# Kernel tuning notes

Hardware: AMD Instinct MI355X
Metric: run time of the kernel (lower is better)

The kernel has to match this reference:

```python
import jax, jax.numpy as jnp
import numpy as np

V, E, H, T = 50000, 300, 512, 16   # vocab, embed_dim, hidden_dim, tagset
Hh = H // 2                         # per-direction LSTM hidden
B, S = 128, 128                     # batch (hardcoded in module), seq_len
START, STOP = 14, 15
NEG = -10000.0


def setup_inputs() -> dict:
    key = jax.random.key(0)
    ks = jax.random.split(key, 16)
    n = lambda k, sh: (jax.random.normal(k, sh, dtype=jnp.float32) * 0.1)
    trans = jax.random.normal(ks[12], (T, T), dtype=jnp.float32)
    trans = trans.at[START, :].set(NEG).at[:, STOP].set(NEG)
    return {
        "sentence": jax.random.randint(ks[0], (B, S), 0, V, dtype=jnp.int32),
        "emb": jax.random.normal(ks[1], (V, E), dtype=jnp.float32),
        "Wih_f": n(ks[2], (4 * Hh, E)), "Whh_f": n(ks[3], (4 * Hh, Hh)),
        "bih_f": n(ks[4], (4 * Hh,)),   "bhh_f": n(ks[5], (4 * Hh,)),
        "Wih_b": n(ks[6], (4 * Hh, E)), "Whh_b": n(ks[7], (4 * Hh, Hh)),
        "bih_b": n(ks[8], (4 * Hh,)),   "bhh_b": n(ks[9], (4 * Hh,)),
        "W_out": n(ks[10], (T, H)),     "b_out": n(ks[11], (T,)),
        "trans": trans,
        "h0": jax.random.normal(ks[13], (2, B, Hh), dtype=jnp.float32),
        "c0": jax.random.normal(ks[14], (2, B, Hh), dtype=jnp.float32),
    }


def _lstm_dir(x_sbE, h0, c0, Wih, Whh, bih, bhh):
    """x_sbE: [S,B,E] -> [S,B,Hh]. PyTorch gate order: i,f,g,o."""
    def cell(carry, xt):
        h, c = carry
        g = xt @ Wih.T + bih + h @ Whh.T + bhh
        i, f, gg, o = jnp.split(g, 4, axis=-1)
        c = jax.nn.sigmoid(f) * c + jax.nn.sigmoid(i) * jnp.tanh(gg)
        h = jax.nn.sigmoid(o) * jnp.tanh(c)
        return (h, c), h
    _, hs = jax.lax.scan(cell, (h0, c0), x_sbE)
    return hs


def _viterbi(feats, trans):
    """Batched Viterbi. feats: [B,S,T]. Returns (scores [B], paths [B,S])."""
    init = jnp.full((B, T), NEG, dtype=feats.dtype).at[:, START].set(0.0)

    def step(fv, feat_t):
        # next_tag_var[b, next, prev] = fv[b, prev] + trans[next, prev]
        nxt = fv[:, None, :] + trans[None, :, :]
        bp = jnp.argmax(nxt, axis=-1)              # [B,T]
        fv = jnp.max(nxt, axis=-1) + feat_t        # [B,T]
        return fv, bp

    fv, bps = jax.lax.scan(step, init, jnp.swapaxes(feats, 0, 1))  # bps: [S,B,T]
    term = fv + trans[STOP][None, :]
    best = jnp.argmax(term, axis=-1)               # [B]
    score = jnp.max(term, axis=-1)                 # [B]

    def back(tag, bp_t):
        prev = jnp.take_along_axis(bp_t, tag[:, None], axis=1)[:, 0]
        return prev, tag

    _, path = jax.lax.scan(back, best, bps, reverse=True)  # [S,B]
    return score, jnp.swapaxes(path, 0, 1)


def reference(sentence, emb, Wih_f, Whh_f, bih_f, bhh_f,
              Wih_b, Whh_b, bih_b, bhh_b, W_out, b_out, trans, h0, c0):
    x = emb[sentence]                               # [B,S,E] (frozen embedding)
    x_sbE = jnp.swapaxes(x, 0, 1)                   # [S,B,E]
    h_f = _lstm_dir(x_sbE, h0[0], c0[0], Wih_f, Whh_f, bih_f, bhh_f)
    h_b = _lstm_dir(x_sbE[::-1], h0[1], c0[1], Wih_b, Whh_b, bih_b, bhh_b)[::-1]
    lstm_out = jnp.concatenate([h_f, h_b], axis=-1)  # [S,B,H]
    feats = jnp.swapaxes(lstm_out @ W_out.T + b_out, 0, 1)  # [B,S,T]
    scores, tag_seqs = _viterbi(feats, trans)
    return scores, tag_seqs
```

## Files before the change

kernel.cpp:

```cpp
#include <hip/hip_runtime.h>
#include <math.h>
#include <stdint.h>

#define BB 128
#define SS 128
#define EE 300
#define HH 256
#define G4 1024
#define TT 16
#define NEGV -10000.0f
#define START_TAG 14
#define STOP_TAG 15

typedef float f32x4 __attribute__((ext_vector_type(4)));
typedef int   i32x4 __attribute__((ext_vector_type(4)));

__device__ __forceinline__ float sigm(float x) { return 1.0f / (1.0f + expf(-x)); }

__device__ __forceinline__ float4 shfl_xor4(float4 v, int m) {
  float4 r;
  r.x = __shfl_xor(v.x, m); r.y = __shfl_xor(v.y, m);
  r.z = __shfl_xor(v.z, m); r.w = __shfl_xor(v.w, m);
  return r;
}
__device__ __forceinline__ void add4(float4& a, const float4& b) {
  a.x += b.x; a.y += b.y; a.z += b.z; a.w += b.w;
}

__device__ __forceinline__ f32x4 load_f4_llc(const float* p) {
  f32x4 v;
  asm volatile("global_load_dwordx4 %0, %1, off sc0 sc1\n\t"
               "s_waitcnt vmcnt(0)"
               : "=v"(v) : "v"(p) : "memory");
  return v;
}
__device__ __forceinline__ void load_tags8(const int* p, i32x4& a, i32x4& b) {
  asm volatile("global_load_dwordx4 %0, %2, off sc0 sc1\n\t"
               "global_load_dwordx4 %1, %2, off offset:16 sc0 sc1\n\t"
               "s_waitcnt vmcnt(0)"
               : "=&v"(a), "=&v"(b) : "v"(p) : "memory");
}

__global__ void k_prep(const float* __restrict__ Wih_f, const float* __restrict__ Whh_f,
                       const float* __restrict__ bih_f, const float* __restrict__ bhh_f,
                       const float* __restrict__ Wih_b, const float* __restrict__ Whh_b,
                       const float* __restrict__ bih_b, const float* __restrict__ bhh_b,
                       float* __restrict__ WihT, float* __restrict__ Whh4,
                       float* __restrict__ bsum, int* __restrict__ ctr) {
  int id = blockIdx.x * blockDim.x + threadIdx.x;
  const int N1 = 2 * EE * G4;
  const int N2 = 2 * HH * G4;
  const int N3 = 2 * G4;
  const int N4 = 64 * 256;
  if (id < N1) {
    int d = id / (EE * G4); int r = id % (EE * G4);
    int e = r / G4; int j = r % G4;
    const float* W = d ? Wih_b : Wih_f;
    WihT[id] = W[j * EE + e];
  } else if (id < N1 + N2) {
    int t = id - N1;
    int d = t / (HH * G4); int r = t % (HH * G4);
    int k = r / G4; int q = r % G4; int u = q >> 2; int g = q & 3;
    const float* W = d ? Whh_b : Whh_f;
    Whh4[t] = W[(g * HH + u) * HH + k];
  } else if (id < N1 + N2 + N3) {
    int t = id - N1 - N2;
    int d = t / G4; int j = t % G4;
    bsum[t] = d ? (bih_b[j] + bhh_b[j]) : (bih_f[j] + bhh_f[j]);
  } else if (id < N1 + N2 + N3 + N4) {
    ctr[id - N1 - N2 - N3] = 0;
  }
}

__global__ void k_xproj(const int* __restrict__ sent, const float* __restrict__ emb,
                        const float* __restrict__ WihT, const float* __restrict__ bsum,
                        float4* __restrict__ xp4) {
  __shared__ __align__(16) float xs[16][EE];
  __shared__ int idxs[16];
  int blk = blockIdx.x;
  int d = blk >> 10;
  int tile = blk & 1023;
  int tid = threadIdx.x;
  if (tid < 16) {
    int sb = tile * 16 + tid;
    int s = sb >> 7, b = sb & 127;
    idxs[tid] = sent[b * SS + s];
  }
  __syncthreads();
  for (int t = tid; t < 16 * 75; t += 256) {
    int i = t / 75, e4 = t % 75;
    ((f32x4*)&xs[i][0])[e4] = ((const f32x4*)(emb + (size_t)idxs[i] * EE))[e4];
  }
  __syncthreads();

  const float* WT = WihT + (size_t)d * EE * G4;
  float acc0[16], acc1[16], acc2[16], acc3[16];
#pragma unroll
  for (int i = 0; i < 16; ++i) { acc0[i] = 0.f; acc1[i] = 0.f; acc2[i] = 0.f; acc3[i] = 0.f; }

  for (int e4 = 0; e4 < 75; ++e4) {
    f32x4 xv[16];
#pragma unroll
    for (int i = 0; i < 16; ++i)
      xv[i] = *(const f32x4*)&xs[i][e4 * 4];
    const float* rowb = WT + (size_t)e4 * 4 * G4;
#pragma unroll
    for (int j = 0; j < 4; ++j) {
      const float* row = rowb + (size_t)j * G4;
      float w0 = row[tid];
      float w1 = row[tid + 256];
      float w2 = row[tid + 512];
      float w3 = row[tid + 768];
#pragma unroll
      for (int i = 0; i < 16; ++i) {
        float x = xv[i][j];
        acc0[i] += w0 * x; acc1[i] += w1 * x; acc2[i] += w2 * x; acc3[i] += w3 * x;
      }
    }
  }
  float b0 = bsum[d * G4 + tid];
  float b1 = bsum[d * G4 + tid + 256];
  float b2 = bsum[d * G4 + tid + 512];
  float b3 = bsum[d * G4 + tid + 768];
#pragma unroll
  for (int i = 0; i < 16; ++i) {
    int sb = tile * 16 + i;
    int s = sb >> 7, b = sb & 127;
    xp4[(((size_t)d * SS + s) * BB + b) * HH + tid] =
        make_float4(acc0[i] + b0, acc1[i] + b1, acc2[i] + b2, acc3[i] + b3);
  }
}

__global__ __launch_bounds__(256, 2) void k_recur(
    const float4* __restrict__ xp4, const float4* __restrict__ Wg,
    const float* __restrict__ Wout, const float* __restrict__ h0,
    const float* __restrict__ c0, float* __restrict__ hbuf,
    float* __restrict__ featsP, int* __restrict__ ctr) {
  __shared__ __align__(16) float hshS[4 * 288];
  __shared__ float hloc[4 * 33];
  __shared__ float WoL[16 * 33];

  int blk = blockIdx.x;
  int d = blk >> 8;
  int bg = (blk >> 3) & 31;
  int sl = blk & 7;
  int bbase = bg * 4;
  int tid = threadIdx.x;
  int u = tid >> 3, kc = tid & 7;
  int uglob = sl * 32 + u;
  int* tagsg = ctr + (d * 32 + bg) * 256 + 64;

  for (int i = tid; i < 16 * 32; i += 256) {
    int t = i >> 5, uu = i & 31;
    WoL[t * 33 + uu] = Wout[t * 512 + d * HH + sl * 32 + uu];
  }

  float4 wreg[32];
  {
    const float4* Wd = Wg + (size_t)d * (HH * HH) + (size_t)(kc * 32) * HH + uglob;
#pragma unroll
    for (int kk = 0; kk < 32; ++kk) wreg[kk] = Wd[(size_t)kk * HH];
  }
  int b_own = ((kc & 1) << 1) | ((kc >> 1) & 1);
  float c_reg = c0[((size_t)d * BB + bbase + b_own) * HH + uglob];
  bool up0 = (kc & 1), up1 = (kc & 2);

  int sb = tid >> 6;
  int sk = (tid & 63) * 4;
  int ldoff = sb * 288 + (sk >> 5) * 36 + (sk & 31);

  for (int step = 0; step < SS; ++step) {
    int s = d ? (SS - 1 - step) : step;
    float4 xg = xp4[(((size_t)d * SS + s) * BB + bbase + b_own) * HH + uglob];

    float* ldst = &hshS[ldoff];
    if (step == 0) {
      const float* ps = h0 + ((size_t)d * BB + bbase + sb) * HH + sk;
      *(f32x4*)ldst = *(const f32x4*)ps;
    } else {
      i32x4 ta, tb;
      int m;
      do {
        load_tags8(tagsg, ta, tb);
        int m0 = min(min(ta[0], ta[1]), min(ta[2], ta[3]));
        int m1 = min(min(tb[0], tb[1]), min(tb[2], tb[3]));
        m = min(m0, m1);
      } while (m < step);
      const float* ps = hbuf + ((size_t)((step - 1) % 3) * 2 + d) * BB * HH +
                        (size_t)(bbase + sb) * HH + sk;
      *(f32x4*)ldst = load_f4_llc(ps);
    }
    __syncthreads();

    float4 a[4];
#pragma unroll
    for (int b = 0; b < 4; ++b) a[b] = make_float4(0.f, 0.f, 0.f, 0.f);
#pragma unroll
    for (int kk4 = 0; kk4 < 8; ++kk4) {
      float hvv[4][4];
#pragma unroll
      for (int b = 0; b < 4; ++b)
        *(f32x4*)&hvv[b][0] = *(const f32x4*)&hshS[b * 288 + kc * 36 + kk4 * 4];
#pragma unroll
      for (int j = 0; j < 4; ++j) {
        float4 w = wreg[kk4 * 4 + j];
#pragma unroll
        for (int b = 0; b < 4; ++b) {
          float hj = hvv[b][j];
          a[b].x += w.x * hj; a[b].y += w.y * hj;
          a[b].z += w.z * hj; a[b].w += w.w * hj;
        }
      }
    }

#pragma unroll
    for (int j = 0; j < 2; ++j) {
      float4 snd = up0 ? a[j] : a[j + 2];
      float4 rcv = shfl_xor4(snd, 1);
      if (!up0) add4(a[j], rcv); else add4(a[j + 2], rcv);
    }
    float4 v0 = up0 ? a[2] : a[0];
    float4 v1 = up0 ? a[3] : a[1];
    {
      float4 snd = up1 ? v0 : v1;
      float4 rcv = shfl_xor4(snd, 2);
      if (!up1) add4(v0, rcv); else add4(v1, rcv);
    }
    float4 keep = up1 ? v1 : v0;
    {
      float4 rcv = shfl_xor4(keep, 4);
      add4(keep, rcv);
    }

    float ii = keep.x + xg.x, ff = keep.y + xg.y;
    float gg = keep.z + xg.z, oo = keep.w + xg.w;
    c_reg = sigm(ff) * c_reg + sigm(ii) * tanhf(gg);
    float hn = sigm(oo) * tanhf(c_reg);

    if (kc < 4) {
      __hip_atomic_store(
          &hbuf[((size_t)(step % 3) * 2 + d) * BB * HH + (size_t)(bbase + b_own) * HH + uglob],
          hn, __ATOMIC_RELAXED, __HIP_MEMORY_SCOPE_AGENT);
      hloc[b_own * 33 + u] = hn;
    }
    __syncthreads();

    if (tid == 0)
      __hip_atomic_store(&tagsg[sl], step + 1, __ATOMIC_RELAXED,
                         __HIP_MEMORY_SCOPE_AGENT);

    {
      int b2 = tid >> 6, t = (tid >> 2) & 15, pr = tid & 3;
      float p = 0.f;
#pragma unroll
      for (int q = 0; q < 8; ++q)
        p += hloc[b2 * 33 + pr * 8 + q] * WoL[t * 33 + pr * 8 + q];
      p += __shfl_xor(p, 1);
      p += __shfl_xor(p, 2);
      if (pr == 0)
        featsP[(((size_t)(d * 8 + sl) * BB + bbase + b2) * SS + s) * TT + t] = p;
    }
  }
}

__global__ void k_fsum(const float* __restrict__ featsP, float* __restrict__ featsF) {
  int b = blockIdx.x;
  int tid = threadIdx.x;
  float acc[8];
#pragma unroll
  for (int j = 0; j < 8; ++j) acc[j] = 0.f;
  for (int dsl = 0; dsl < 16; ++dsl) {
    const float* fp = featsP + ((size_t)dsl * BB + b) * (SS * TT);
#pragma unroll
    for (int j = 0; j < 8; ++j) acc[j] += fp[j * 256 + tid];
  }
  float* fo = featsF + (size_t)b * (SS * TT);
#pragma unroll
  for (int j = 0; j < 8; ++j) fo[j * 256 + tid] = acc[j];
}

__global__ void k_viterbi(const float* __restrict__ featsF, const float* __restrict__ b_out,
                          const float* __restrict__ trans, float* __restrict__ out) {
  __shared__ float tr[TT * TT];
  __shared__ unsigned char bpl[16][SS][TT];
  int tid = threadIdx.x;
  if (tid < TT * TT) tr[tid] = trans[tid];
  __syncthreads();

  int bg = tid >> 4;
  int next = tid & 15;
  int b = blockIdx.x * 16 + bg;
  float fv = (next == START_TAG) ? 0.0f : NEGV;
  float bo = b_out[next];
  const float* fF = featsF + (size_t)b * SS * TT;

  for (int s = 0; s < SS; ++s) {
    float best = -INFINITY; int arg = 0;
#pragma unroll
    for (int prev = 0; prev < TT; ++prev) {
      float fvp = __shfl(fv, prev, 16);
      float cand = fvp + tr[next * TT + prev];
      if (cand > best) { best = cand; arg = prev; }
    }
    float feat = fF[s * TT + next] + bo;
    fv = best + feat;
    bpl[bg][s][next] = (unsigned char)arg;
  }

  float bv = fv + tr[STOP_TAG * TT + next];
  int bi = next;
#pragma unroll
  for (int off = 8; off; off >>= 1) {
    float ov = __shfl_down(bv, off, 16);
    int oi = __shfl_down(bi, off, 16);
    if (ov > bv || (ov == bv && oi < bi)) { bv = ov; bi = oi; }
  }
  if (next == 0) {
    out[b] = bv;
    int tag = bi;
    float* po = out + BB + (size_t)b * SS;
    for (int s = SS - 1; s >= 0; --s) {
      po[s] = (float)tag;
      tag = bpl[bg][s][tag];
    }
  }
}

extern "C" void kernel_launch(void* const* d_in, const int* in_sizes, int n_in,
                              void* d_out, int out_size, void* d_ws, size_t ws_size,
                              hipStream_t stream) {
  const int*   sent  = (const int*)d_in[0];
  const float* emb   = (const float*)d_in[1];
  const float* Wih_f = (const float*)d_in[2];
  const float* Whh_f = (const float*)d_in[3];
  const float* bih_f = (const float*)d_in[4];
  const float* bhh_f = (const float*)d_in[5];
  const float* Wih_b = (const float*)d_in[6];
  const float* Whh_b = (const float*)d_in[7];
  const float* bih_b = (const float*)d_in[8];
  const float* bhh_b = (const float*)d_in[9];
  const float* Wout  = (const float*)d_in[10];
  const float* b_out = (const float*)d_in[11];
  const float* trans = (const float*)d_in[12];
  const float* h0    = (const float*)d_in[13];
  const float* c0    = (const float*)d_in[14];

  float* ws = (float*)d_ws;
  size_t off = 0;
  float* xproj  = ws + off; off += (size_t)2 * SS * BB * G4;
  float* WihT   = ws + off; off += (size_t)2 * EE * G4;
  float* Whh4   = ws + off; off += (size_t)2 * HH * G4;
  float* bsum   = ws + off; off += (size_t)2 * G4;
  float* featsP = ws + off; off += (size_t)16 * BB * SS * TT;
  float* featsF = ws + off; off += (size_t)BB * SS * TT;
  float* hbuf   = ws + off; off += (size_t)3 * 2 * BB * HH;
  int*   ctr    = (int*)(ws + off); off += 64 * 256;

  const int NPREP = 2 * EE * G4 + 2 * HH * G4 + 2 * G4 + 64 * 256;
  k_prep<<<(NPREP + 255) / 256, 256, 0, stream>>>(Wih_f, Whh_f, bih_f, bhh_f,
                                                  Wih_b, Whh_b, bih_b, bhh_b,
                                                  WihT, Whh4, bsum, ctr);
  k_xproj<<<2048, 256, 0, stream>>>(sent, emb, WihT, bsum, (float4*)xproj);

  {
    const float4* xp4c = (const float4*)xproj;
    const float4* Wgc  = (const float4*)Whh4;
    void* kargs[] = {(void*)&xp4c, (void*)&Wgc, (void*)&Wout, (void*)&h0,
                     (void*)&c0, (void*)&hbuf, (void*)&featsP, (void*)&ctr};
    hipError_t e = hipLaunchCooperativeKernel(k_recur, dim3(512), dim3(256),
                                              kargs, 0, stream);
    if (e != hipSuccess) {
      k_recur<<<512, 256, 0, stream>>>(xp4c, Wgc, Wout, h0, c0, hbuf, featsP, ctr);
    }
  }

  k_fsum<<<BB, 256, 0, stream>>>(featsP, featsF);
  k_viterbi<<<8, 256, 0, stream>>>(featsF, b_out, trans, (float*)d_out);
}
```

Baseline: 841.3 us.

## Replace tag-counter sync with stamped h-value pairs and move output projection out

Each hidden value is now stored together with its step stamp as one 64-bit atomic. Consumers spin on the stamps directly instead of first polling per-slice counters and then loading hbuf, which removes a round trip and a block barrier from the serial recurrence. The h tile in shared memory is double-buffered, which removes the second __syncthreads per step. The per-step output projection and the fsum pass are replaced by storing all h values and running a separate k_feats GEMV kernel, at the cost of extra memory traffic and one more kernel.

```diff
diff --git a/kernel.cpp b/kernel.cpp
--- a/kernel.cpp
+++ b/kernel.cpp
@@ -13,7 +13,6 @@
 #define STOP_TAG 15
 
 typedef float f32x4 __attribute__((ext_vector_type(4)));
-typedef int   i32x4 __attribute__((ext_vector_type(4)));
 
 __device__ __forceinline__ float sigm(float x) { return 1.0f / (1.0f + expf(-x)); }
 
@@ -27,18 +26,16 @@
   a.x += b.x; a.y += b.y; a.z += b.z; a.w += b.w;
 }
 
-__device__ __forceinline__ f32x4 load_f4_llc(const float* p) {
-  f32x4 v;
-  asm volatile("global_load_dwordx4 %0, %1, off sc0 sc1\n\t"
-               "s_waitcnt vmcnt(0)"
-               : "=v"(v) : "v"(p) : "memory");
-  return v;
-}
-__device__ __forceinline__ void load_tags8(const int* p, i32x4& a, i32x4& b) {
+__device__ __forceinline__ void load_pairs8(const float* p, f32x4& a, f32x4& b) {
   asm volatile("global_load_dwordx4 %0, %2, off sc0 sc1\n\t"
                "global_load_dwordx4 %1, %2, off offset:16 sc0 sc1\n\t"
                "s_waitcnt vmcnt(0)"
                : "=&v"(a), "=&v"(b) : "v"(p) : "memory");
+}
+
+__device__ __forceinline__ void store_pair_llc(float2* p, float h, int stamp) {
+  uint64_t bits = ((uint64_t)(uint32_t)stamp << 32) | (uint64_t)__float_as_uint(h);
+  __hip_atomic_store((uint64_t*)p, bits, __ATOMIC_RELAXED, __HIP_MEMORY_SCOPE_AGENT);
 }
 
 __global__ void k_prep(const float* __restrict__ Wih_f, const float* __restrict__ Whh_f,
@@ -46,12 +43,12 @@
                        const float* __restrict__ Wih_b, const float* __restrict__ Whh_b,
                        const float* __restrict__ bih_b, const float* __restrict__ bhh_b,
                        float* __restrict__ WihT, float* __restrict__ Whh4,
-                       float* __restrict__ bsum, int* __restrict__ ctr) {
+                       float* __restrict__ bsum, float* __restrict__ hpairz) {
   int id = blockIdx.x * blockDim.x + threadIdx.x;
   const int N1 = 2 * EE * G4;
   const int N2 = 2 * HH * G4;
   const int N3 = 2 * G4;
-  const int N4 = 64 * 256;
+  const int N4 = 3 * 2 * BB * HH * 2;
   if (id < N1) {
     int d = id / (EE * G4); int r = id % (EE * G4);
     int e = r / G4; int j = r % G4;
@@ -68,7 +65,7 @@
     int d = t / G4; int j = t % G4;
     bsum[t] = d ? (bih_b[j] + bhh_b[j]) : (bih_f[j] + bhh_f[j]);
   } else if (id < N1 + N2 + N3 + N4) {
-    ctr[id - N1 - N2 - N3] = 0;
+    hpairz[id - N1 - N2 - N3] = 0.0f;
   }
 }
 
@@ -133,12 +130,9 @@
 
 __global__ __launch_bounds__(256, 2) void k_recur(
     const float4* __restrict__ xp4, const float4* __restrict__ Wg,
-    const float* __restrict__ Wout, const float* __restrict__ h0,
-    const float* __restrict__ c0, float* __restrict__ hbuf,
-    float* __restrict__ featsP, int* __restrict__ ctr) {
-  __shared__ __align__(16) float hshS[4 * 288];
-  __shared__ float hloc[4 * 33];
-  __shared__ float WoL[16 * 33];
+    const float* __restrict__ h0, const float* __restrict__ c0,
+    float2* __restrict__ hpair, float* __restrict__ hall) {
+  __shared__ __align__(16) float hsh[2][4 * 288];
 
   int blk = blockIdx.x;
   int d = blk >> 8;
@@ -148,12 +142,6 @@
   int tid = threadIdx.x;
   int u = tid >> 3, kc = tid & 7;
   int uglob = sl * 32 + u;
-  int* tagsg = ctr + (d * 32 + bg) * 256 + 64;
-
-  for (int i = tid; i < 16 * 32; i += 256) {
-    int t = i >> 5, uu = i & 31;
-    WoL[t * 33 + uu] = Wout[t * 512 + d * HH + sl * 32 + uu];
-  }
 
   float4 wreg[32];
   {
@@ -166,32 +154,35 @@
   bool up0 = (kc & 1), up1 = (kc & 2);
 
   int sb = tid >> 6;
-  int sk = (tid & 63) * 4;
-  int ldoff = sb * 288 + (sk >> 5) * 36 + (sk & 31);
+  int k4 = (tid & 63) * 4;
+  int ldoff = sb * 288 + (k4 >> 5) * 36 + (k4 & 31);
 
   for (int step = 0; step < SS; ++step) {
     int s = d ? (SS - 1 - step) : step;
+    int pb = step & 1;
     float4 xg = xp4[(((size_t)d * SS + s) * BB + bbase + b_own) * HH + uglob];
 
-    float* ldst = &hshS[ldoff];
+    float* ldst = &hsh[pb][ldoff];
     if (step == 0) {
-      const float* ps = h0 + ((size_t)d * BB + bbase + sb) * HH + sk;
+      const float* ps = h0 + ((size_t)d * BB + bbase + sb) * HH + k4;
       *(f32x4*)ldst = *(const f32x4*)ps;
     } else {
-      i32x4 ta, tb;
-      int m;
-      do {
-        load_tags8(tagsg, ta, tb);
-        int m0 = min(min(ta[0], ta[1]), min(ta[2], ta[3]));
-        int m1 = min(min(tb[0], tb[1]), min(tb[2], tb[3]));
-        m = min(m0, m1);
-      } while (m < step);
-      const float* ps = hbuf + ((size_t)((step - 1) % 3) * 2 + d) * BB * HH +
-                        (size_t)(bbase + sb) * HH + sk;
-      *(f32x4*)ldst = load_f4_llc(ps);
+      int slot_r = (step + 2) % 3;
+      const float* ps = (const float*)(hpair +
+          ((size_t)(slot_r * 2 + d) * BB + bbase + sb) * HH + k4);
+      f32x4 v0, v1;
+      load_pairs8(ps, v0, v1);
+      while (__float_as_int(v0[1]) != step || __float_as_int(v0[3]) != step ||
+             __float_as_int(v1[1]) != step || __float_as_int(v1[3]) != step) {
+        __builtin_amdgcn_s_sleep(1);
+        load_pairs8(ps, v0, v1);
+      }
+      f32x4 q = {v0[0], v0[2], v1[0], v1[2]};
+      *(f32x4*)ldst = q;
     }
     __syncthreads();
 
+    const float* hb = &hsh[pb][0];
     float4 a[4];
 #pragma unroll
     for (int b = 0; b < 4; ++b) a[b] = make_float4(0.f, 0.f, 0.f, 0.f);
@@ -200,7 +191,7 @@
       float hvv[4][4];
 #pragma unroll
       for (int b = 0; b < 4; ++b)
-        *(f32x4*)&hvv[b][0] = *(const f32x4*)&hshS[b * 288 + kc * 36 + kk4 * 4];
+        *(f32x4*)&hvv[b][0] = *(const f32x4*)&hb[b * 288 + kc * 36 + kk4 * 4];
 #pragma unroll
       for (int j = 0; j < 4; ++j) {
         float4 w = wreg[kk4 * 4 + j];
@@ -238,45 +229,41 @@
     float hn = sigm(oo) * tanhf(c_reg);
 
     if (kc < 4) {
-      __hip_atomic_store(
-          &hbuf[((size_t)(step % 3) * 2 + d) * BB * HH + (size_t)(bbase + b_own) * HH + uglob],
-          hn, __ATOMIC_RELAXED, __HIP_MEMORY_SCOPE_AGENT);
-      hloc[b_own * 33 + u] = hn;
-    }
-    __syncthreads();
-
-    if (tid == 0)
-      __hip_atomic_store(&tagsg[sl], step + 1, __ATOMIC_RELAXED,
-                         __HIP_MEMORY_SCOPE_AGENT);
-
-    {
-      int b2 = tid >> 6, t = (tid >> 2) & 15, pr = tid & 3;
-      float p = 0.f;
-#pragma unroll
-      for (int q = 0; q < 8; ++q)
-        p += hloc[b2 * 33 + pr * 8 + q] * WoL[t * 33 + pr * 8 + q];
-      p += __shfl_xor(p, 1);
-      p += __shfl_xor(p, 2);
-      if (pr == 0)
-        featsP[(((size_t)(d * 8 + sl) * BB + bbase + b2) * SS + s) * TT + t] = p;
-    }
-  }
-}
-
-__global__ void k_fsum(const float* __restrict__ featsP, float* __restrict__ featsF) {
-  int b = blockIdx.x;
+      store_pair_llc(&hpair[((size_t)((step % 3) * 2 + d) * BB + bbase + b_own) * HH + uglob],
+                     hn, step + 1);
+      hall[(((size_t)d * SS + step) * BB + bbase + b_own) * HH + uglob] = hn;
+    }
+  }
+}
+
+__global__ void k_feats(const float* __restrict__ hall, const float* __restrict__ Wout,
+                        float* __restrict__ featsF) {
+  __shared__ __align__(16) float h2[16][516];
+  int b = blockIdx.x >> 3;
+  int sg = blockIdx.x & 7;
   int tid = threadIdx.x;
-  float acc[8];
-#pragma unroll
-  for (int j = 0; j < 8; ++j) acc[j] = 0.f;
-  for (int dsl = 0; dsl < 16; ++dsl) {
-    const float* fp = featsP + ((size_t)dsl * BB + b) * (SS * TT);
-#pragma unroll
-    for (int j = 0; j < 8; ++j) acc[j] += fp[j * 256 + tid];
-  }
-  float* fo = featsF + (size_t)b * (SS * TT);
-#pragma unroll
-  for (int j = 0; j < 8; ++j) fo[j * 256 + tid] = acc[j];
+
+  for (int i = tid; i < 16 * 128; i += 256) {
+    int r = i >> 7, seg = i & 127;
+    int s = sg * 16 + r;
+    f32x4 v;
+    if (seg < 64)
+      v = *(const f32x4*)&hall[(((size_t)0 * SS + s) * BB + b) * HH + seg * 4];
+    else
+      v = *(const f32x4*)&hall[(((size_t)1 * SS + (SS - 1 - s)) * BB + b) * HH + (seg - 64) * 4];
+    *(f32x4*)&h2[r][seg * 4] = v;
+  }
+  __syncthreads();
+
+  int sloc = tid >> 4, t = tid & 15;
+  const float* wrow = Wout + t * 512;
+  float p = 0.f;
+  for (int j = 0; j < 128; ++j) {
+    f32x4 hv = *(const f32x4*)&h2[sloc][j * 4];
+    f32x4 wv = *(const f32x4*)&wrow[j * 4];
+    p += hv[0] * wv[0] + hv[1] * wv[1] + hv[2] * wv[2] + hv[3] * wv[3];
+  }
+  featsF[((size_t)b * SS + sg * 16 + sloc) * TT + t] = p;
 }
 
 __global__ void k_viterbi(const float* __restrict__ featsF, const float* __restrict__ b_out,
@@ -351,29 +338,29 @@
   float* WihT   = ws + off; off += (size_t)2 * EE * G4;
   float* Whh4   = ws + off; off += (size_t)2 * HH * G4;
   float* bsum   = ws + off; off += (size_t)2 * G4;
-  float* featsP = ws + off; off += (size_t)16 * BB * SS * TT;
   float* featsF = ws + off; off += (size_t)BB * SS * TT;
-  float* hbuf   = ws + off; off += (size_t)3 * 2 * BB * HH;
-  int*   ctr    = (int*)(ws + off); off += 64 * 256;
-
-  const int NPREP = 2 * EE * G4 + 2 * HH * G4 + 2 * G4 + 64 * 256;
+  float* hall   = ws + off; off += (size_t)2 * SS * BB * HH;
+  float* hpairf = ws + off; off += (size_t)3 * 2 * BB * HH * 2;
+
+  const int NPREP = 2 * EE * G4 + 2 * HH * G4 + 2 * G4 + 3 * 2 * BB * HH * 2;
   k_prep<<<(NPREP + 255) / 256, 256, 0, stream>>>(Wih_f, Whh_f, bih_f, bhh_f,
                                                   Wih_b, Whh_b, bih_b, bhh_b,
-                                                  WihT, Whh4, bsum, ctr);
+                                                  WihT, Whh4, bsum, hpairf);
   k_xproj<<<2048, 256, 0, stream>>>(sent, emb, WihT, bsum, (float4*)xproj);
 
   {
     const float4* xp4c = (const float4*)xproj;
     const float4* Wgc  = (const float4*)Whh4;
-    void* kargs[] = {(void*)&xp4c, (void*)&Wgc, (void*)&Wout, (void*)&h0,
-                     (void*)&c0, (void*)&hbuf, (void*)&featsP, (void*)&ctr};
+    float2* hpair = (float2*)hpairf;
+    void* kargs[] = {(void*)&xp4c, (void*)&Wgc, (void*)&h0, (void*)&c0,
+                     (void*)&hpair, (void*)&hall};
     hipError_t e = hipLaunchCooperativeKernel(k_recur, dim3(512), dim3(256),
                                               kargs, 0, stream);
     if (e != hipSuccess) {
-      k_recur<<<512, 256, 0, stream>>>(xp4c, Wgc, Wout, h0, c0, hbuf, featsP, ctr);
-    }
-  }
-
-  k_fsum<<<BB, 256, 0, stream>>>(featsP, featsF);
+      k_recur<<<512, 256, 0, stream>>>(xp4c, Wgc, h0, c0, hpair, hall);
+    }
+  }
+
+  k_feats<<<1024, 256, 0, stream>>>(hall, Wout, featsF);
   k_viterbi<<<8, 256, 0, stream>>>(featsF, b_out, trans, (float*)d_out);
 }
```

Result: slower. 909.0 us (+8.1%).
